# Kernel tuning notes

Measured on AMD Instinct MI355X. Metric: run time of the kernel, lower is better.

The kernel has to match this reference:

```python
import jax, jax.numpy as jnp
import numpy as np

DIM = 192
NUM_TOKENS = 64
RD = 10
B, N = 32, 4096
EPS = 1e-12  # F.normalize eps


def setup_inputs() -> dict:
    key = jax.random.key(0)
    ks = jax.random.split(key, 9)
    s = 1.0 / np.sqrt(DIM)
    return {
        "x": jax.random.normal(ks[0], (B, N, DIM), dtype=jnp.float32),
        "td": jax.random.normal(ks[1], (B, NUM_TOKENS, DIM), dtype=jnp.float32),
        "wq_w": jax.random.uniform(ks[2], (RD, DIM), jnp.float32, -s, s),
        "wq_b": jax.random.uniform(ks[3], (RD,), jnp.float32, -s, s),
        "wk_w": jax.random.uniform(ks[4], (RD, DIM), jnp.float32, -s, s),
        "wk_b": jax.random.uniform(ks[5], (RD,), jnp.float32, -s, s),
        "wv_w": jax.random.uniform(ks[6], (DIM, DIM), jnp.float32, -s, s),
        "wv_b": jax.random.uniform(ks[7], (DIM,), jnp.float32, -s, s),
        "scale": jnp.ones((1,), dtype=jnp.float32),
        "x_size": 64,
    }


def _l2norm(t):
    # matches F.normalize(dim=-1, eps=1e-12): x / max(||x||, eps)
    n = jnp.sqrt(jnp.sum(t * t, axis=-1, keepdims=True))
    return t / jnp.maximum(n, EPS)


def reference(x, td, wq_w, wq_b, wk_w, wk_b, wv_w, wv_b, scale, x_size):
    # q: (b, n, dr); k: (b, m, dr); v: (b, m, c)
    q = jnp.einsum("bnc,dc->bnd", x, wq_w) + wq_b
    k = jnp.einsum("bmc,dc->bmd", td, wk_w) + wk_b
    v = jnp.einsum("bmc,ec->bme", td, wv_w) + wv_b
    # cosine similarity attention logits: (b, n, m)
    attn = jnp.einsum("bnd,bmd->bnm", _l2norm(q), _l2norm(k))
    attn = attn * (1.0 + jnp.clip(scale, 0.0, 3.0) * np.log(NUM_TOKENS))
    attn = jax.nn.softmax(attn, axis=-1)
    out = jnp.einsum("bnm,bme->bne", attn, v)  # (b, n, c)
    return out, attn
```

## Files before the change

kernel.cpp:

```cpp
#include <hip/hip_runtime.h>
#include <math.h>

#define DIM 192
#define NT 64
#define RD 10
#define BB 32
#define NN 4096
#define LN64 4.1588830833596715f

typedef __attribute__((ext_vector_type(8))) short short8v;
typedef __attribute__((ext_vector_type(4))) float float4v;

#define WQF_OFF 0
#define KNF_OFF 4096
#define VF_OFF  (4096 + 32 * 2048)

__device__ __forceinline__ ushort f2bf(float f) {
    union { float f; unsigned u; } v; v.f = f;
    unsigned r = (v.u + 0x7fffu + ((v.u >> 16) & 1u)) >> 16;
    return (ushort)r;
}

__global__ __launch_bounds__(256, 2) void ATD_prep(
        const float* __restrict__ td,
        const float* __restrict__ wk_w, const float* __restrict__ wk_b,
        const float* __restrict__ wv_w, const float* __restrict__ wv_b,
        const float* __restrict__ wq_w,
        ushort* __restrict__ wsu) {
    __shared__ float smem[15696];
    const int b = blockIdx.x, y = blockIdx.y, t = threadIdx.x;
    const float* tdb = td + (size_t)b * NT * DIM;

    if (y < 12) {
        float4* td_s = (float4*)smem;
        float4* wv_s = (float4*)(smem + 64 * 196);
        float*  wvb_s = smem + 64 * 196 + 16 * 196;

        const float4* tds = (const float4*)tdb;
        #pragma unroll
        for (int j = 0; j < 12; ++j) {
            int idx = t + 256 * j;
            td_s[(idx / 48) * 49 + (idx % 48)] = tds[idx];
        }
        const float4* wvs = (const float4*)(wv_w + (size_t)(y * 16) * DIM);
        #pragma unroll
        for (int j = 0; j < 3; ++j) {
            int idx = t + 256 * j;
            wv_s[(idx / 48) * 49 + (idx % 48)] = wvs[idx];
        }
        if (t < 16) wvb_s[t] = wv_b[y * 16 + t];
        __syncthreads();

        const int ks = t >> 7;
        const int l  = (t >> 1) & 63;
        const int ih = t & 1;
        const int mb = ks * 32 + (l >> 4) * 8 + ih * 4;
        const int e  = l & 15;

        float a0 = wvb_s[e], a1 = a0, a2 = a0, a3 = a0;
        const float4* w4 = wv_s + e * 49;
        const float4* t0 = td_s + (mb + 0) * 49;
        const float4* t1 = td_s + (mb + 1) * 49;
        const float4* t2 = td_s + (mb + 2) * 49;
        const float4* t3 = td_s + (mb + 3) * 49;
        #pragma unroll 4
        for (int c4 = 0; c4 < 48; ++c4) {
            float4 w = w4[c4];
            float4 r0 = t0[c4], r1 = t1[c4], r2 = t2[c4], r3 = t3[c4];
            a0 += r0.x * w.x + r0.y * w.y + r0.z * w.z + r0.w * w.w;
            a1 += r1.x * w.x + r1.y * w.y + r1.z * w.z + r1.w * w.w;
            a2 += r2.x * w.x + r2.y * w.y + r2.z * w.z + r2.w * w.w;
            a3 += r3.x * w.x + r3.y * w.y + r3.z * w.z + r3.w * w.w;
        }
        ushort o[4] = {f2bf(a0), f2bf(a1), f2bf(a2), f2bf(a3)};
        *(uint2*)(wsu + VF_OFF + (size_t)b * 12288 + ks * 6144 + y * 512 + l * 8 + ih * 4)
            = *(uint2*)o;
    } else {
        float* kp   = smem;
        float* kn_s = smem + 3072;

        const int m = t & 63, ch = t >> 6;
        float k[RD];
        #pragma unroll
        for (int d = 0; d < RD; ++d) k[d] = 0.f;
        const float4* td4 = (const float4*)(tdb + (size_t)m * DIM) + ch * 12;
        #pragma unroll 4
        for (int c4 = 0; c4 < 12; ++c4) {
            float4 a = td4[c4];
            #pragma unroll
            for (int d = 0; d < RD; ++d) {
                float4 w = ((const float4*)(wk_w + (size_t)d * DIM))[ch * 12 + c4];
                k[d] += a.x * w.x + a.y * w.y + a.z * w.z + a.w * w.w;
            }
        }
        #pragma unroll
        for (int d = 0; d < RD; ++d) kp[(ch * 64 + m) * 12 + d] = k[d];
        __syncthreads();
        if (t < NT) {
            float kk[RD], ss = 0.f;
            #pragma unroll
            for (int d = 0; d < RD; ++d) {
                kk[d] = wk_b[d] + kp[t * 12 + d] + kp[(64 + t) * 12 + d]
                      + kp[(128 + t) * 12 + d] + kp[(192 + t) * 12 + d];
                ss += kk[d] * kk[d];
            }
            float rn = 1.f / fmaxf(sqrtf(ss), 1e-12f);
            #pragma unroll
            for (int d = 0; d < 16; ++d)
                kn_s[t * 16 + d] = (d < RD) ? kk[d] * rn : 0.f;
        }
        __syncthreads();
        {
            int mt = t >> 6, l = t & 63;
            ushort tmp[8];
            #pragma unroll
            for (int i = 0; i < 8; ++i) {
                int d = (l >> 4) * 8 + i;
                int mm = mt * 16 + (l & 15);
                tmp[i] = (d < 16) ? f2bf(kn_s[mm * 16 + d]) : (ushort)0;
            }
            *(uint4*)(wsu + KNF_OFF + (size_t)b * 2048 + t * 8) = *(uint4*)tmp;
        }
        if (b == 0) {
            for (int s = t; s < 384; s += 256) {
                int ksq = s >> 6, l = s & 63;
                ushort tmp[8];
                #pragma unroll
                for (int i = 0; i < 8; ++i) {
                    int d = l & 15;
                    int c = ksq * 32 + (l >> 4) * 8 + i;
                    tmp[i] = (d < RD) ? f2bf(wq_w[(size_t)d * DIM + c]) : (ushort)0;
                }
                *(uint4*)(wsu + WQF_OFF + s * 8) = *(uint4*)tmp;
            }
        }
    }
}

__global__ __launch_bounds__(256, 4) void ATD_main(
        const float* __restrict__ x, const float* __restrict__ wq_b,
        const float* __restrict__ scale, const ushort* __restrict__ wsu,
        float* __restrict__ out, float* __restrict__ attn) {
    __shared__ ushort qn_lds[4][512];
    __shared__ ushort p_lds[4][1024];

    const int t = threadIdx.x, w = t >> 6, l = t & 63;
    const int b = blockIdx.y;
    const int rbase = blockIdx.x * 64 + w * 16;
    const int lg = l >> 4;
    const int lc = l & 15;

    float4 xf[12];
    {
        const float* xr = x + ((size_t)b * NN + rbase + lc) * DIM + lg * 8;
        #pragma unroll
        for (int ks = 0; ks < 6; ++ks) {
            xf[2 * ks]     = *(const float4*)(xr + ks * 32);
            xf[2 * ks + 1] = *(const float4*)(xr + ks * 32 + 4);
        }
    }

    short8v wqf[6];
    #pragma unroll
    for (int ks = 0; ks < 6; ++ks)
        wqf[ks] = *(const short8v*)(wsu + WQF_OFF + ks * 512 + l * 8);
    short8v knf[4];
    #pragma unroll
    for (int mt = 0; mt < 4; ++mt)
        knf[mt] = *(const short8v*)(wsu + KNF_OFF + (size_t)b * 2048 + mt * 512 + l * 8);

    {
        unsigned* z = (unsigned*)(&qn_lds[w][0]);
        #pragma unroll
        for (int i = 0; i < 4; ++i) z[l + 64 * i] = 0u;
    }

    const float bias = (lc < RD) ? wq_b[lc] : 0.f;
    const float factor = 1.0f + fminf(fmaxf(scale[0], 0.f), 3.f) * LN64;

    char* qnbase = (char*)(&qn_lds[w][0]);
    char* pbase  = (char*)(&p_lds[w][0]);
    const float4v z4 = {0.f, 0.f, 0.f, 0.f};

    float4v qacc = {bias, bias, bias, bias};
    #pragma unroll
    for (int ks = 0; ks < 6; ++ks) {
        float xv[8] = {xf[2 * ks].x, xf[2 * ks].y, xf[2 * ks].z, xf[2 * ks].w,
                       xf[2 * ks + 1].x, xf[2 * ks + 1].y, xf[2 * ks + 1].z, xf[2 * ks + 1].w};
        unsigned hi[4], lo[4];
        #pragma unroll
        for (int i = 0; i < 4; ++i) {
            unsigned a = __float_as_uint(xv[2 * i]);
            unsigned c = __float_as_uint(xv[2 * i + 1]);
            hi[i] = (a >> 16) | (c & 0xFFFF0000u);
            float h0 = __uint_as_float(a & 0xFFFF0000u);
            float h1 = __uint_as_float(c & 0xFFFF0000u);
            float d0 = xv[2 * i] - h0;
            float d1 = xv[2 * i + 1] - h1;
            lo[i] = (__float_as_uint(d0) >> 16) | (__float_as_uint(d1) & 0xFFFF0000u);
        }
        short8v xhi = *(short8v*)hi;
        short8v xlo = *(short8v*)lo;
        qacc = __builtin_amdgcn_mfma_f32_16x16x32_bf16(xhi, wqf[ks], qacc, 0, 0, 0);
        qacc = __builtin_amdgcn_mfma_f32_16x16x32_bf16(xlo, wqf[ks], qacc, 0, 0, 0);
    }

    float sj[4];
    #pragma unroll
    for (int j = 0; j < 4; ++j) sj[j] = qacc[j] * qacc[j];
    #pragma unroll
    for (int mm = 1; mm < 16; mm <<= 1) {
        #pragma unroll
        for (int j = 0; j < 4; ++j) sj[j] += __shfl_xor(sj[j], mm, 64);
    }
    #pragma unroll
    for (int j = 0; j < 4; ++j) {
        float rn = 1.f / fmaxf(sqrtf(sj[j]), 1e-12f);
        int row = lg * 4 + j;
        int addr = (row * 64 + lc * 2) ^ (((row >> 2) & 3) << 5);
        *(ushort*)(qnbase + addr) = f2bf(qacc[j] * rn);
    }

    float4v sA[4];
    {
        int aaddr = (lc * 64 + lg * 16) ^ (((lc >> 2) & 3) << 5);
        short8v qnB = *(short8v*)(qnbase + aaddr);
        #pragma unroll
        for (int mt = 0; mt < 4; ++mt)
            sA[mt] = __builtin_amdgcn_mfma_f32_16x16x32_bf16(knf[mt], qnB, z4, 0, 0, 0);
    }

    float pv[4][4];
    {
        float mx = sA[0][0];
        #pragma unroll
        for (int mt = 0; mt < 4; ++mt)
            #pragma unroll
            for (int j = 0; j < 4; ++j) mx = fmaxf(mx, sA[mt][j]);
        mx = fmaxf(mx, __shfl_xor(mx, 16, 64));
        mx = fmaxf(mx, __shfl_xor(mx, 32, 64));
        float sum = 0.f;
        #pragma unroll
        for (int mt = 0; mt < 4; ++mt)
            #pragma unroll
            for (int j = 0; j < 4; ++j) {
                float e = __expf((sA[mt][j] - mx) * factor);
                pv[mt][j] = e; sum += e;
            }
        sum += __shfl_xor(sum, 16, 64);
        sum += __shfl_xor(sum, 32, 64);
        float inv = 1.f / sum;
        #pragma unroll
        for (int mt = 0; mt < 4; ++mt)
            #pragma unroll
            for (int j = 0; j < 4; ++j) pv[mt][j] *= inv;
    }

    #pragma unroll
    for (int mt = 0; mt < 4; ++mt) {
        ushort pk[4] = {f2bf(pv[mt][0]), f2bf(pv[mt][1]),
                        f2bf(pv[mt][2]), f2bf(pv[mt][3])};
        int addr = (lc * 128 + mt * 32 + lg * 8) ^ ((lc & 7) << 4);
        *(uint2*)(pbase + addr) = *(uint2*)pk;
    }

    {
        float* ab = attn + ((size_t)b * NN + rbase + lc) * NT;
        #pragma unroll
        for (int mt = 0; mt < 4; ++mt) {
            float4 v4 = make_float4(pv[mt][0], pv[mt][1], pv[mt][2], pv[mt][3]);
            *(float4*)(ab + mt * 16 + lg * 4) = v4;
        }
    }

    {
        const ushort* vfb = wsu + VF_OFF + (size_t)b * 12288;
        short8v pB0 = *(short8v*)(pbase + ((lc * 128 + lg * 16) ^ ((lc & 7) << 4)));
        short8v pB1 = *(short8v*)(pbase + ((lc * 128 + 64 + lg * 16) ^ ((lc & 7) << 4)));
        float* ob = out + ((size_t)b * NN + rbase + lc) * DIM;

        short8v A0 = *(const short8v*)(vfb + l * 8);
        short8v A1 = *(const short8v*)(vfb + 6144 + l * 8);
        #pragma unroll
        for (int ct = 0; ct < 12; ++ct) {
            short8v nA0 = A0, nA1 = A1;
            if (ct < 11) {
                nA0 = *(const short8v*)(vfb + (ct + 1) * 512 + l * 8);
                nA1 = *(const short8v*)(vfb + 6144 + (ct + 1) * 512 + l * 8);
            }
            float4v acc = __builtin_amdgcn_mfma_f32_16x16x32_bf16(A0, pB0, z4, 0, 0, 0);
            acc = __builtin_amdgcn_mfma_f32_16x16x32_bf16(A1, pB1, acc, 0, 0, 0);
            float4 o4 = make_float4(acc[0], acc[1], acc[2], acc[3]);
            *(float4*)(ob + ct * 16 + lg * 4) = o4;
            A0 = nA0; A1 = nA1;
        }
    }
}

extern "C" void kernel_launch(void* const* d_in, const int* in_sizes, int n_in,
                              void* d_out, int out_size, void* d_ws, size_t ws_size,
                              hipStream_t stream) {
    const float* x     = (const float*)d_in[0];
    const float* td    = (const float*)d_in[1];
    const float* wq_w  = (const float*)d_in[2];
    const float* wq_b  = (const float*)d_in[3];
    const float* wk_w  = (const float*)d_in[4];
    const float* wk_b  = (const float*)d_in[5];
    const float* wv_w  = (const float*)d_in[6];
    const float* wv_b  = (const float*)d_in[7];
    const float* scale = (const float*)d_in[8];

    float* out  = (float*)d_out;
    float* attn = out + (size_t)BB * NN * DIM;
    ushort* wsu = (ushort*)d_ws;

    ATD_prep<<<dim3(BB, 13), 256, 0, stream>>>(td, wk_w, wk_b, wv_w, wv_b, wq_w, wsu);
    ATD_main<<<dim3(NN / 64, BB), 256, 0, stream>>>(x, wq_b, scale, wsu, out, attn);
}
```

Baseline: 56.71 us.

## Process two row tiles per block, prefetching second x tile during first

Each block now handles 128 rows instead of 64. It loads the x tile for the second half while the first half's normalization, softmax and PV compute run, with a sched_barrier keeping the prefetch ahead. Per-batch K/Wq fragments are reused across both tiles. Output and attention stores become nontemporal and the attn store is moved after the out store. The extra live x registers may reduce occupancy, and the grid is halved.

```diff
diff --git a/kernel.cpp b/kernel.cpp
--- a/kernel.cpp
+++ b/kernel.cpp
@@ -137,51 +137,16 @@
     }
 }
 
-__global__ __launch_bounds__(256, 4) void ATD_main(
-        const float* __restrict__ x, const float* __restrict__ wq_b,
-        const float* __restrict__ scale, const ushort* __restrict__ wsu,
-        float* __restrict__ out, float* __restrict__ attn) {
-    __shared__ ushort qn_lds[4][512];
-    __shared__ ushort p_lds[4][1024];
-
-    const int t = threadIdx.x, w = t >> 6, l = t & 63;
-    const int b = blockIdx.y;
-    const int rbase = blockIdx.x * 64 + w * 16;
-    const int lg = l >> 4;
-    const int lc = l & 15;
-
-    float4 xf[12];
-    {
-        const float* xr = x + ((size_t)b * NN + rbase + lc) * DIM + lg * 8;
-        #pragma unroll
-        for (int ks = 0; ks < 6; ++ks) {
-            xf[2 * ks]     = *(const float4*)(xr + ks * 32);
-            xf[2 * ks + 1] = *(const float4*)(xr + ks * 32 + 4);
-        }
-    }
-
-    short8v wqf[6];
-    #pragma unroll
-    for (int ks = 0; ks < 6; ++ks)
-        wqf[ks] = *(const short8v*)(wsu + WQF_OFF + ks * 512 + l * 8);
-    short8v knf[4];
-    #pragma unroll
-    for (int mt = 0; mt < 4; ++mt)
-        knf[mt] = *(const short8v*)(wsu + KNF_OFF + (size_t)b * 2048 + mt * 512 + l * 8);
-
-    {
-        unsigned* z = (unsigned*)(&qn_lds[w][0]);
-        #pragma unroll
-        for (int i = 0; i < 4; ++i) z[l + 64 * i] = 0u;
-    }
-
-    const float bias = (lc < RD) ? wq_b[lc] : 0.f;
-    const float factor = 1.0f + fminf(fmaxf(scale[0], 0.f), 3.f) * LN64;
-
-    char* qnbase = (char*)(&qn_lds[w][0]);
-    char* pbase  = (char*)(&p_lds[w][0]);
-    const float4v z4 = {0.f, 0.f, 0.f, 0.f};
-
+__device__ __forceinline__ void load_x(float4 (&xf)[12], const float* xr) {
+    #pragma unroll
+    for (int ks = 0; ks < 6; ++ks) {
+        xf[2 * ks]     = *(const float4*)(xr + ks * 32);
+        xf[2 * ks + 1] = *(const float4*)(xr + ks * 32 + 4);
+    }
+}
+
+__device__ __forceinline__ float4v do_qproj(const float4 (&xf)[12],
+                                            const short8v (&wqf)[6], float bias) {
     float4v qacc = {bias, bias, bias, bias};
     #pragma unroll
     for (int ks = 0; ks < 6; ++ks) {
@@ -204,6 +169,15 @@
         qacc = __builtin_amdgcn_mfma_f32_16x16x32_bf16(xhi, wqf[ks], qacc, 0, 0, 0);
         qacc = __builtin_amdgcn_mfma_f32_16x16x32_bf16(xlo, wqf[ks], qacc, 0, 0, 0);
     }
+    return qacc;
+}
+
+__device__ __forceinline__ void tile_tail(float4v qacc, int b, int rbase,
+        int l, int lg, int lc, char* qnbase, char* pbase,
+        const short8v (&knf)[4], float factor,
+        const ushort* __restrict__ vfb,
+        float* __restrict__ out, float* __restrict__ attn) {
+    const float4v z4 = {0.f, 0.f, 0.f, 0.f};
 
     float sj[4];
     #pragma unroll
@@ -265,16 +239,6 @@
     }
 
     {
-        float* ab = attn + ((size_t)b * NN + rbase + lc) * NT;
-        #pragma unroll
-        for (int mt = 0; mt < 4; ++mt) {
-            float4 v4 = make_float4(pv[mt][0], pv[mt][1], pv[mt][2], pv[mt][3]);
-            *(float4*)(ab + mt * 16 + lg * 4) = v4;
-        }
-    }
-
-    {
-        const ushort* vfb = wsu + VF_OFF + (size_t)b * 12288;
         short8v pB0 = *(short8v*)(pbase + ((lc * 128 + lg * 16) ^ ((lc & 7) << 4)));
         short8v pB1 = *(short8v*)(pbase + ((lc * 128 + 64 + lg * 16) ^ ((lc & 7) << 4)));
         float* ob = out + ((size_t)b * NN + rbase + lc) * DIM;
@@ -290,11 +254,70 @@
             }
             float4v acc = __builtin_amdgcn_mfma_f32_16x16x32_bf16(A0, pB0, z4, 0, 0, 0);
             acc = __builtin_amdgcn_mfma_f32_16x16x32_bf16(A1, pB1, acc, 0, 0, 0);
-            float4 o4 = make_float4(acc[0], acc[1], acc[2], acc[3]);
-            *(float4*)(ob + ct * 16 + lg * 4) = o4;
+            __builtin_nontemporal_store(acc, (float4v*)(ob + ct * 16 + lg * 4));
             A0 = nA0; A1 = nA1;
         }
     }
+
+    {
+        float* ab = attn + ((size_t)b * NN + rbase + lc) * NT;
+        #pragma unroll
+        for (int mt = 0; mt < 4; ++mt) {
+            float4v v4 = {pv[mt][0], pv[mt][1], pv[mt][2], pv[mt][3]};
+            __builtin_nontemporal_store(v4, (float4v*)(ab + mt * 16 + lg * 4));
+        }
+    }
+}
+
+__global__ __launch_bounds__(256, 4) void ATD_main(
+        const float* __restrict__ x, const float* __restrict__ wq_b,
+        const float* __restrict__ scale, const ushort* __restrict__ wsu,
+        float* __restrict__ out, float* __restrict__ attn) {
+    __shared__ ushort qn_lds[4][512];
+    __shared__ ushort p_lds[4][1024];
+
+    const int t = threadIdx.x, w = t >> 6, l = t & 63;
+    const int b = blockIdx.y;
+    const int rbase0 = blockIdx.x * 128 + w * 16;
+    const int rbase1 = rbase0 + 64;
+    const int lg = l >> 4;
+    const int lc = l & 15;
+
+    float4 xfA[12];
+    load_x(xfA, x + ((size_t)b * NN + rbase0 + lc) * DIM + lg * 8);
+
+    short8v wqf[6];
+    #pragma unroll
+    for (int ks = 0; ks < 6; ++ks)
+        wqf[ks] = *(const short8v*)(wsu + WQF_OFF + ks * 512 + l * 8);
+    short8v knf[4];
+    #pragma unroll
+    for (int mt = 0; mt < 4; ++mt)
+        knf[mt] = *(const short8v*)(wsu + KNF_OFF + (size_t)b * 2048 + mt * 512 + l * 8);
+
+    {
+        unsigned* z = (unsigned*)(&qn_lds[w][0]);
+        #pragma unroll
+        for (int i = 0; i < 4; ++i) z[l + 64 * i] = 0u;
+    }
+
+    const float bias = (lc < RD) ? wq_b[lc] : 0.f;
+    const float factor = 1.0f + fminf(fmaxf(scale[0], 0.f), 3.f) * LN64;
+
+    char* qnbase = (char*)(&qn_lds[w][0]);
+    char* pbase  = (char*)(&p_lds[w][0]);
+    const ushort* vfb = wsu + VF_OFF + (size_t)b * 12288;
+
+    float4v q0 = do_qproj(xfA, wqf, bias);
+
+    float4 xfB[12];
+    load_x(xfB, x + ((size_t)b * NN + rbase1 + lc) * DIM + lg * 8);
+    __builtin_amdgcn_sched_barrier(0);
+
+    tile_tail(q0, b, rbase0, l, lg, lc, qnbase, pbase, knf, factor, vfb, out, attn);
+
+    float4v q1 = do_qproj(xfB, wqf, bias);
+    tile_tail(q1, b, rbase1, l, lg, lc, qnbase, pbase, knf, factor, vfb, out, attn);
 }
 
 extern "C" void kernel_launch(void* const* d_in, const int* in_sizes, int n_in,
@@ -315,5 +338,5 @@
     ushort* wsu = (ushort*)d_ws;
 
     ATD_prep<<<dim3(BB, 13), 256, 0, stream>>>(td, wk_w, wk_b, wv_w, wv_b, wq_w, wsu);
-    ATD_main<<<dim3(NN / 64, BB), 256, 0, stream>>>(x, wq_b, scale, wsu, out, attn);
-}
+    ATD_main<<<dim3(NN / 128, BB), 256, 0, stream>>>(x, wq_b, scale, wsu, out, attn);
+}
```

New measurement: 78.96 us. 1.39x slower.
